# Optimization experiments

Hardware: AMD Instinct MI355X
Metric: run time of the kernel (lower is better)

Reference implementation:

```python
import jax, jax.numpy as jnp
import numpy as np

N_ATOM = 2_000_000
N_FRAG = 200_000
EPS = 1e-4


def setup_inputs() -> dict:
    key = jax.random.key(0)
    k1, k2, k3, k4, k5 = jax.random.split(key, 5)
    f_atom = jax.random.normal(k1, (N_ATOM, 3), dtype=jnp.float32)
    atom_pos = jax.random.normal(k2, (N_ATOM, 3), dtype=jnp.float32) * 5.0
    T_frag = jax.random.normal(k3, (N_FRAG, 3), dtype=jnp.float32) * 5.0
    frag_id = jax.random.randint(k4, (N_ATOM,), 0, N_FRAG, dtype=jnp.int32)
    frag_sizes = jax.random.randint(k5, (N_FRAG,), 0, 30, dtype=jnp.int32)
    return {
        "f_atom": f_atom,
        "atom_pos": atom_pos,
        "T_frag": T_frag,
        "frag_id": frag_id,
        "n_frag": N_FRAG,
        "frag_sizes": frag_sizes,
    }


def reference(f_atom, atom_pos, T_frag, frag_id, n_frag, frag_sizes):
    """Newton-Euler aggregation: per-atom forces -> fragment (v, omega)."""
    seg = lambda x: jax.ops.segment_sum(x, frag_id, num_segments=n_frag)

    # scatter_mean of forces -> translational velocity [n_frag, 3]
    counts = seg(jnp.ones((f_atom.shape[0],), dtype=f_atom.dtype))  # [n_frag]
    v_frag = seg(f_atom) / jnp.maximum(counts, 1.0)[:, None]

    # lever arms and torques
    r_arm = atom_pos - T_frag[frag_id]                 # [N_atom, 3]
    torque = seg(jnp.cross(r_arm, f_atom))            # [n_frag, 3]

    # inertia tensor: I = sum(r^2) * eye - sum(r r^T)  (+ eps regularization)
    r2 = jnp.sum(r_arm * r_arm, axis=-1)              # [N_atom]
    I_diag = seg(r2)                                   # [n_frag]
    I_off = seg(r_arm[:, :, None] * r_arm[:, None, :])  # [n_frag, 3, 3]
    eye3 = jnp.eye(3, dtype=f_atom.dtype)
    I_tensor = I_diag[:, None, None] * eye3 - I_off + EPS * eye3

    # batched 3x3 solve for angular velocity
    omega_frag = jnp.linalg.solve(I_tensor, torque[..., None])[..., 0]

    # zero omega for single-atom fragments
    single_mask = (frag_sizes <= 1)[:, None]
    omega_frag = jnp.where(single_mask, jnp.zeros_like(omega_frag), omega_frag)
    return v_frag, omega_frag
```

## Files before the change

### kernel.cpp

```cpp
#include <hip/hip_runtime.h>


#define BSHIFT 9
#define BFRAGS (1 << BSHIFT)
#define NBMAX  512
#define NACC   13

#define CHUNK     4096
#define B_THREADS 512
#define TILE_B    1024
#define R_THREADS 512
#define TILE      1024

__global__ void atom_accum_kernel(const float* __restrict__ f_atom,
                                  const float* __restrict__ atom_pos,
                                  const float* __restrict__ T_frag,
                                  const int*   __restrict__ frag_id,
                                  float* __restrict__ acc,
                                  int n_atom, int n_frag) {
    int i = blockIdx.x * blockDim.x + threadIdx.x;
    if (i >= n_atom) return;
    float fx = f_atom[3 * i + 0], fy = f_atom[3 * i + 1], fz = f_atom[3 * i + 2];
    float px = atom_pos[3 * i + 0], py = atom_pos[3 * i + 1], pz = atom_pos[3 * i + 2];
    int fid = frag_id[i];
    float rx = px - T_frag[3 * fid + 0];
    float ry = py - T_frag[3 * fid + 1];
    float rz = pz - T_frag[3 * fid + 2];
    atomicAdd(&acc[0 * n_frag + fid], 1.0f);
    atomicAdd(&acc[1 * n_frag + fid], fx);
    atomicAdd(&acc[2 * n_frag + fid], fy);
    atomicAdd(&acc[3 * n_frag + fid], fz);
    atomicAdd(&acc[4 * n_frag + fid], ry * fz - rz * fy);
    atomicAdd(&acc[5 * n_frag + fid], rz * fx - rx * fz);
    atomicAdd(&acc[6 * n_frag + fid], rx * fy - ry * fx);
    atomicAdd(&acc[7 * n_frag + fid], rx * rx);
    atomicAdd(&acc[8 * n_frag + fid], ry * ry);
    atomicAdd(&acc[9 * n_frag + fid], rz * rz);
    atomicAdd(&acc[10 * n_frag + fid], rx * ry);
    atomicAdd(&acc[11 * n_frag + fid], rx * rz);
    atomicAdd(&acc[12 * n_frag + fid], ry * rz);
}

__device__ __forceinline__ void solve_frag(const float s[NACC], int fs,
                                           float* vout, float* oout) {
    float inv_cnt = 1.0f / fmaxf(s[0], 1.0f);
    vout[0] = s[1] * inv_cnt;
    vout[1] = s[2] * inv_cnt;
    vout[2] = s[3] * inv_cnt;

    double sxx = (double)s[7], syy = (double)s[8], szz = (double)s[9];
    double sxy = (double)s[10], sxz = (double)s[11], syz = (double)s[12];
    const double eps = 1e-4;
    double d = sxx + syy + szz;
    double a00 = d - sxx + eps, a11 = d - syy + eps, a22 = d - szz + eps;
    double a01 = -sxy, a02 = -sxz, a12 = -syz;

    double c00 = a11 * a22 - a12 * a12;
    double c01 = a02 * a12 - a01 * a22;
    double c02 = a01 * a12 - a02 * a11;
    double det = a00 * c00 + a01 * c01 + a02 * c02;
    double inv_det = (det != 0.0) ? 1.0 / det : 0.0;
    double c11 = a00 * a22 - a02 * a02;
    double c12 = a01 * a02 - a00 * a12;
    double c22 = a00 * a11 - a01 * a01;

    double tx = (double)s[4], ty = (double)s[5], tz = (double)s[6];
    if (fs <= 1) {
        oout[0] = 0.0f; oout[1] = 0.0f; oout[2] = 0.0f;
    } else {
        oout[0] = (float)((c00 * tx + c01 * ty + c02 * tz) * inv_det);
        oout[1] = (float)((c01 * tx + c11 * ty + c12 * tz) * inv_det);
        oout[2] = (float)((c02 * tx + c12 * ty + c22 * tz) * inv_det);
    }
}

__global__ void finalize_accum_kernel(const float* __restrict__ acc,
                                      const int* __restrict__ frag_sizes,
                                      float* __restrict__ out, int n_frag) {
    int i = blockIdx.x * blockDim.x + threadIdx.x;
    if (i >= n_frag) return;
    float s[NACC];
#pragma unroll
    for (int c = 0; c < NACC; ++c) s[c] = acc[(size_t)c * n_frag + i];
    float v[3], o[3];
    solve_frag(s, frag_sizes[i], v, o);
    out[3 * i + 0] = v[0]; out[3 * i + 1] = v[1]; out[3 * i + 2] = v[2];
    float* om = out + 3 * (size_t)n_frag;
    om[3 * i + 0] = o[0]; om[3 * i + 1] = o[1]; om[3 * i + 2] = o[2];
}


__device__ __forceinline__ int xcd_swizzle(int orig, int n) {
    int q = n >> 3, r = n & 7;
    int xcd = orig & 7, slot = orig >> 3;
    return (xcd < r ? xcd * (q + 1) : r * (q + 1) + (xcd - r) * q) + slot;
}

__global__ __launch_bounds__(B_THREADS)
void hist_kernel(const int* __restrict__ frag_id, unsigned* __restrict__ h,
                 int n_atom, int nb) {
    __shared__ unsigned hh[NBMAX];
    int tid = threadIdx.x;
    if (tid < nb) hh[tid] = 0;
    __syncthreads();
    int c0 = blockIdx.x * CHUNK;
    int cend = min(c0 + CHUNK, n_atom);
    for (int i = c0 + tid; i < cend; i += B_THREADS)
        atomicAdd(&hh[frag_id[i] >> BSHIFT], 1u);
    __syncthreads();
    size_t row = (size_t)blockIdx.x * nb;
    if (tid < nb) h[row + tid] = hh[tid];
}

__global__ void colscan_kernel(unsigned* __restrict__ h, unsigned* __restrict__ T,
                               int nb, int nreg) {
    int wid = (blockIdx.x * blockDim.x + threadIdx.x) >> 6;
    int lane = threadIdx.x & 63;
    if (wid >= nb) return;
    unsigned run = 0;
    for (int k0 = 0; k0 < nreg; k0 += 64) {
        int k = k0 + lane;
        unsigned v = (k < nreg) ? h[(size_t)k * nb + wid] : 0u;
        unsigned incl = v;
#pragma unroll
        for (int o = 1; o < 64; o <<= 1) {
            unsigned x = __shfl_up(incl, o);
            if (lane >= o) incl += x;
        }
        if (k < nreg) h[(size_t)k * nb + wid] = run + (incl - v);
        run += __shfl(incl, 63);
    }
    if (lane == 0) T[wid] = run;
}

__global__ __launch_bounds__(1024)
void gscan_kernel(const unsigned* __restrict__ T, unsigned* __restrict__ gstart,
                  int nb) {
    __shared__ unsigned s[1024];
    int t = threadIdx.x;
    unsigned v = (t < nb) ? T[t] : 0u;
    s[t] = v;
    __syncthreads();
    for (int o = 1; o < 1024; o <<= 1) {
        unsigned x = (t >= o) ? s[t - o] : 0u;
        __syncthreads();
        s[t] += x;
        __syncthreads();
    }
    if (t < nb) gstart[t] = s[t] - v;
    if (t == 0) gstart[nb] = s[nb - 1];
}

__global__ __launch_bounds__(B_THREADS)
void build_kernel(const float* __restrict__ f_atom,
                  const float* __restrict__ atom_pos,
                  const float* __restrict__ T_frag,
                  const int* __restrict__ frag_id,
                  const unsigned* __restrict__ h,
                  const unsigned* __restrict__ gstart,
                  float* __restrict__ payload,
                  int n_atom, int nb, int nreg) {
    __shared__ float stage[TILE_B * 8];
    __shared__ unsigned cursor[NBMAX];
    __shared__ unsigned cnt[NBMAX];
    __shared__ unsigned tfs[NBMAX + 1];
    __shared__ unsigned wsum[B_THREADS / 64];

    int tid = threadIdx.x;
    int wave = tid >> 6, lane = tid & 63;
    int blk = xcd_swizzle(blockIdx.x, nreg);

    size_t row = (size_t)blk * nb;
    if (tid < nb) cursor[tid] = gstart[tid] + h[row + tid];

    int c0 = blk * CHUNK;
    int cend = min(c0 + CHUNK, n_atom);

    for (int tbase = c0; tbase < cend; tbase += TILE_B) {
        int tcount = min(TILE_B, cend - tbase);
        cnt[tid] = 0;
        __syncthreads();

        float4 p0j[2], p1j[2];
        unsigned rankj[2]; int bj[2]; bool actj[2];
#pragma unroll
        for (int j = 0; j < 2; ++j) {
            int i = tbase + tid + j * B_THREADS;
            actj[j] = (i < cend);
            bj[j] = 0; rankj[j] = 0;
            if (actj[j]) {
                int fid = frag_id[i];
                int b = fid >> BSHIFT;
                bj[j] = b;
                rankj[j] = atomicAdd(&cnt[b], 1u);
                float fx = f_atom[3 * i + 0], fy = f_atom[3 * i + 1],
                      fz = f_atom[3 * i + 2];
                float rx = atom_pos[3 * i + 0] - T_frag[3 * fid + 0];
                float ry = atom_pos[3 * i + 1] - T_frag[3 * fid + 1];
                float rz = atom_pos[3 * i + 2] - T_frag[3 * fid + 2];
                p0j[j] = make_float4(fx, fy, fz, __int_as_float(fid));
                p1j[j] = make_float4(rx, ry, rz, 0.0f);
            }
        }
        __syncthreads();

        unsigned v = cnt[tid];
        unsigned incl = v;
#pragma unroll
        for (int o = 1; o < 64; o <<= 1) {
            unsigned x = __shfl_up(incl, o);
            if (lane >= o) incl += x;
        }
        if (lane == 63) wsum[wave] = incl;
        __syncthreads();
        unsigned wbase = 0;
#pragma unroll
        for (int w = 0; w < B_THREADS / 64; ++w)
            wbase += (w < wave) ? wsum[w] : 0u;
        tfs[tid] = wbase + incl - v;
        if (tid == B_THREADS - 1) tfs[NBMAX] = wbase + incl;
        __syncthreads();

#pragma unroll
        for (int j = 0; j < 2; ++j) {
            if (actj[j]) {
                unsigned slot = tfs[bj[j]] + rankj[j];
                unsigned dst = cursor[bj[j]] + rankj[j];
                p1j[j].w = __uint_as_float(dst);
                float4* d = (float4*)&stage[(size_t)slot * 8];
                d[0] = p0j[j];
                d[1] = p1j[j];
            }
        }
        __syncthreads();

        for (int s = tid; s < tcount; s += B_THREADS) {
            const float4* q = (const float4*)&stage[(size_t)s * 8];
            float4 a = q[0];
            float4 c = q[1];
            unsigned dst = __float_as_uint(c.w);
            float4* p = (float4*)(payload + (size_t)dst * 8);
            p[0] = a;
            p[1] = c;
        }
        if (tid < nb) cursor[tid] += cnt[tid];
    }
}

__global__ __launch_bounds__(R_THREADS)
void reduce_kernel(const float* __restrict__ payload,
                   const unsigned* __restrict__ gstart,
                   const int* __restrict__ frag_sizes,
                   float* __restrict__ out, int n_frag, int nb) {
    __shared__ float stage[TILE * 8];
    __shared__ unsigned cnt[BFRAGS];
    __shared__ unsigned fstart[BFRAGS + 1];
    __shared__ unsigned wsum[R_THREADS / 64];

    int b = xcd_swizzle(blockIdx.x, nb);
    int tid = threadIdx.x;
    int wave = tid >> 6, lane = tid & 63;
    unsigned s0 = gstart[b], s1 = gstart[b + 1];

    float m0 = 0.f, m1 = 0.f, m2 = 0.f, m3 = 0.f, m4 = 0.f, m5 = 0.f,
          m6 = 0.f, m7 = 0.f, m8 = 0.f, m9 = 0.f, m10 = 0.f, m11 = 0.f,
          m12 = 0.f;

    for (unsigned tbase = s0; tbase < s1; tbase += TILE) {
        cnt[tid] = 0;
        __syncthreads();

        float4 p0j[2], p1j[2];
        unsigned rankj[2]; int lfj[2]; bool actj[2];
#pragma unroll
        for (int j = 0; j < 2; ++j) {
            unsigned s = tbase + (unsigned)tid + (unsigned)j * R_THREADS;
            actj[j] = (s < s1);
            lfj[j] = 0; rankj[j] = 0;
            if (actj[j]) {
                const float4* p = (const float4*)(payload + (size_t)s * 8);
                p0j[j] = p[0];
                p1j[j] = p[1];
                lfj[j] = __float_as_int(p0j[j].w) & (BFRAGS - 1);
                rankj[j] = atomicAdd(&cnt[lfj[j]], 1u);
            }
        }
        __syncthreads();

        unsigned v = cnt[tid];
        unsigned incl = v;
#pragma unroll
        for (int o = 1; o < 64; o <<= 1) {
            unsigned x = __shfl_up(incl, o);
            if (lane >= o) incl += x;
        }
        if (lane == 63) wsum[wave] = incl;
        __syncthreads();
        unsigned wbase = 0;
#pragma unroll
        for (int w = 0; w < R_THREADS / 64; ++w)
            wbase += (w < wave) ? wsum[w] : 0u;
        fstart[tid] = wbase + incl - v;
        if (tid == R_THREADS - 1) fstart[BFRAGS] = wbase + incl;
        __syncthreads();

#pragma unroll
        for (int j = 0; j < 2; ++j) {
            if (actj[j]) {
                unsigned slot = fstart[lfj[j]] + rankj[j];
                float4* d = (float4*)&stage[(size_t)slot * 8];
                d[0] = p0j[j];
                d[1] = p1j[j];
            }
        }
        __syncthreads();

        unsigned e0 = fstart[tid], e1 = fstart[tid + 1];
        for (unsigned u = e0; u < e1; ++u) {
            const float4* q = (const float4*)&stage[(size_t)u * 8];
            float4 a = q[0];
            float4 c = q[1];
            float fx = a.x, fy = a.y, fz = a.z;
            float rx = c.x, ry = c.y, rz = c.z;
            m0 += 1.0f;
            m1 += fx; m2 += fy; m3 += fz;
            m4 += ry * fz - rz * fy;
            m5 += rz * fx - rx * fz;
            m6 += rx * fy - ry * fx;
            m7 += rx * rx; m8 += ry * ry; m9 += rz * rz;
            m10 += rx * ry; m11 += rx * rz; m12 += ry * rz;
        }
    }

    int fid = (b << BSHIFT) + tid;
    if (fid < n_frag) {
        float sv[NACC] = {m0, m1, m2, m3, m4, m5, m6,
                          m7, m8, m9, m10, m11, m12};
        float v[3], o[3];
        solve_frag(sv, frag_sizes[fid], v, o);
        out[3 * fid + 0] = v[0];
        out[3 * fid + 1] = v[1];
        out[3 * fid + 2] = v[2];
        float* om = out + 3 * (size_t)n_frag;
        om[3 * fid + 0] = o[0];
        om[3 * fid + 1] = o[1];
        om[3 * fid + 2] = o[2];
    }
}


static inline size_t pad256(size_t x) { return (x + 255) & ~(size_t)255; }

extern "C" void kernel_launch(void* const* d_in, const int* in_sizes, int n_in,
                              void* d_out, int out_size, void* d_ws, size_t ws_size,
                              hipStream_t stream) {
    const float* f_atom   = (const float*)d_in[0];
    const float* atom_pos = (const float*)d_in[1];
    const float* T_frag   = (const float*)d_in[2];
    const int*   frag_id  = (const int*)d_in[3];
    const int*   frag_sizes = (const int*)d_in[5];

    int n_atom = in_sizes[0] / 3;
    int n_frag = in_sizes[2] / 3;
    int nb   = (n_frag + BFRAGS - 1) >> BSHIFT;
    int nreg = (n_atom + CHUNK - 1) / CHUNK;

    size_t h_bytes   = pad256((size_t)nreg * nb * sizeof(unsigned));
    size_t ctl_bytes = pad256(((size_t)nb + (size_t)nb + 1) * sizeof(unsigned));
    size_t payload_bytes = (size_t)n_atom * 8 * sizeof(float);
    bool sorted_ok = (nb <= NBMAX) &&
                     (h_bytes + ctl_bytes + payload_bytes <= ws_size);

    if (sorted_ok) {
        unsigned* h      = (unsigned*)d_ws;
        unsigned* T      = (unsigned*)((char*)d_ws + h_bytes);
        unsigned* gstart = T + nb;
        float* payload   = (float*)((char*)d_ws + h_bytes + ctl_bytes);

        hist_kernel<<<nreg, B_THREADS, 0, stream>>>(frag_id, h, n_atom, nb);
        int cs_blocks = (nb * 64 + 255) / 256;
        colscan_kernel<<<cs_blocks, 256, 0, stream>>>(h, T, nb, nreg);
        gscan_kernel<<<1, 1024, 0, stream>>>(T, gstart, nb);
        build_kernel<<<nreg, B_THREADS, 0, stream>>>(f_atom, atom_pos, T_frag,
                                                     frag_id, h, gstart, payload,
                                                     n_atom, nb, nreg);
        reduce_kernel<<<nb, R_THREADS, 0, stream>>>(payload, gstart, frag_sizes,
                                                    (float*)d_out, n_frag, nb);
    } else {
        float* acc = (float*)d_ws;
        hipMemsetAsync(acc, 0, (size_t)NACC * n_frag * sizeof(float), stream);
        int threads = 256;
        atom_accum_kernel<<<(n_atom + threads - 1) / threads, threads, 0, stream>>>(
            f_atom, atom_pos, T_frag, frag_id, acc, n_atom, n_frag);
        finalize_accum_kernel<<<(n_frag + threads - 1) / threads, threads, 0, stream>>>(
            acc, frag_sizes, (float*)d_out, n_frag);
    }
}
```

Baseline: 90.43 us.

## Widen fragment buckets to 1024 and process 1536-atom tiles in counting sort

```diff
diff --git a/kernel.cpp b/kernel.cpp
--- a/kernel.cpp
+++ b/kernel.cpp
@@ -1,16 +1,17 @@
 #include <hip/hip_runtime.h>
 
 
-#define BSHIFT 9
+#define BSHIFT 10
 #define BFRAGS (1 << BSHIFT)
-#define NBMAX  512
+#define NBMAX  256
 #define NACC   13
 
-#define CHUNK     4096
+#define TILE_B    1536
+#define NTILES    3
+#define CHUNK     (TILE_B * NTILES)
 #define B_THREADS 512
-#define TILE_B    1024
 #define R_THREADS 512
-#define TILE      1024
+#define TILE      1536
 
 __global__ void atom_accum_kernel(const float* __restrict__ f_atom,
                                   const float* __restrict__ atom_pos,
@@ -101,7 +102,7 @@
                  int n_atom, int nb) {
     __shared__ unsigned hh[NBMAX];
     int tid = threadIdx.x;
-    if (tid < nb) hh[tid] = 0;
+    if (tid < NBMAX) hh[tid] = 0;
     __syncthreads();
     int c0 = blockIdx.x * CHUNK;
     int cend = min(c0 + CHUNK, n_atom);
@@ -163,11 +164,11 @@
     __shared__ float stage[TILE_B * 8];
     __shared__ unsigned cursor[NBMAX];
     __shared__ unsigned cnt[NBMAX];
-    __shared__ unsigned tfs[NBMAX + 1];
-    __shared__ unsigned wsum[B_THREADS / 64];
+    __shared__ unsigned tfs[NBMAX];
+    __shared__ unsigned wsum[NBMAX / 64];
 
     int tid = threadIdx.x;
-    int wave = tid >> 6, lane = tid & 63;
+    int lane = tid & 63;
     int blk = xcd_swizzle(blockIdx.x, nreg);
 
     size_t row = (size_t)blk * nb;
@@ -178,13 +179,13 @@
 
     for (int tbase = c0; tbase < cend; tbase += TILE_B) {
         int tcount = min(TILE_B, cend - tbase);
-        cnt[tid] = 0;
-        __syncthreads();
-
-        float4 p0j[2], p1j[2];
-        unsigned rankj[2]; int bj[2]; bool actj[2];
-#pragma unroll
-        for (int j = 0; j < 2; ++j) {
+        if (tid < NBMAX) cnt[tid] = 0;
+        __syncthreads();
+
+        float4 p0j[3], p1j[3];
+        unsigned rankj[3]; int bj[3]; bool actj[3];
+#pragma unroll
+        for (int j = 0; j < 3; ++j) {
             int i = tbase + tid + j * B_THREADS;
             actj[j] = (i < cend);
             bj[j] = 0; rankj[j] = 0;
@@ -198,35 +199,37 @@
                 float rx = atom_pos[3 * i + 0] - T_frag[3 * fid + 0];
                 float ry = atom_pos[3 * i + 1] - T_frag[3 * fid + 1];
                 float rz = atom_pos[3 * i + 2] - T_frag[3 * fid + 2];
+                unsigned dst = cursor[b] + rankj[j];
                 p0j[j] = make_float4(fx, fy, fz, __int_as_float(fid));
-                p1j[j] = make_float4(rx, ry, rz, 0.0f);
+                p1j[j] = make_float4(rx, ry, rz, __uint_as_float(dst));
             }
         }
         __syncthreads();
 
-        unsigned v = cnt[tid];
-        unsigned incl = v;
-#pragma unroll
-        for (int o = 1; o < 64; o <<= 1) {
-            unsigned x = __shfl_up(incl, o);
-            if (lane >= o) incl += x;
-        }
-        if (lane == 63) wsum[wave] = incl;
-        __syncthreads();
-        unsigned wbase = 0;
-#pragma unroll
-        for (int w = 0; w < B_THREADS / 64; ++w)
-            wbase += (w < wave) ? wsum[w] : 0u;
-        tfs[tid] = wbase + incl - v;
-        if (tid == B_THREADS - 1) tfs[NBMAX] = wbase + incl;
-        __syncthreads();
-
-#pragma unroll
-        for (int j = 0; j < 2; ++j) {
+        if (tid < NBMAX) {
+            unsigned v = cnt[tid];
+            unsigned incl = v;
+#pragma unroll
+            for (int o = 1; o < 64; o <<= 1) {
+                unsigned x = __shfl_up(incl, o);
+                if (lane >= o) incl += x;
+            }
+            if (lane == 63) wsum[tid >> 6] = incl;
+            __syncthreads();
+            unsigned wbase = 0;
+#pragma unroll
+            for (int w = 0; w < NBMAX / 64; ++w)
+                wbase += (w < (tid >> 6)) ? wsum[w] : 0u;
+            tfs[tid] = wbase + incl - v;
+        } else {
+            __syncthreads();
+        }
+        __syncthreads();
+
+#pragma unroll
+        for (int j = 0; j < 3; ++j) {
             if (actj[j]) {
                 unsigned slot = tfs[bj[j]] + rankj[j];
-                unsigned dst = cursor[bj[j]] + rankj[j];
-                p1j[j].w = __uint_as_float(dst);
                 float4* d = (float4*)&stage[(size_t)slot * 8];
                 d[0] = p0j[j];
                 d[1] = p1j[j];
@@ -254,7 +257,6 @@
                    float* __restrict__ out, int n_frag, int nb) {
     __shared__ float stage[TILE * 8];
     __shared__ unsigned cnt[BFRAGS];
-    __shared__ unsigned fstart[BFRAGS + 1];
     __shared__ unsigned wsum[R_THREADS / 64];
 
     int b = xcd_swizzle(blockIdx.x, nb);
@@ -262,18 +264,20 @@
     int wave = tid >> 6, lane = tid & 63;
     unsigned s0 = gstart[b], s1 = gstart[b + 1];
 
-    float m0 = 0.f, m1 = 0.f, m2 = 0.f, m3 = 0.f, m4 = 0.f, m5 = 0.f,
-          m6 = 0.f, m7 = 0.f, m8 = 0.f, m9 = 0.f, m10 = 0.f, m11 = 0.f,
-          m12 = 0.f;
+    float a0 = 0.f, a1 = 0.f, a2 = 0.f, a3 = 0.f, a4 = 0.f, a5 = 0.f, a6 = 0.f,
+          a7 = 0.f, a8 = 0.f, a9 = 0.f, a10 = 0.f, a11 = 0.f, a12 = 0.f;
+    float b0 = 0.f, b1 = 0.f, b2 = 0.f, b3 = 0.f, b4 = 0.f, b5 = 0.f, b6 = 0.f,
+          b7 = 0.f, b8 = 0.f, b9 = 0.f, b10 = 0.f, b11 = 0.f, b12 = 0.f;
 
     for (unsigned tbase = s0; tbase < s1; tbase += TILE) {
         cnt[tid] = 0;
-        __syncthreads();
-
-        float4 p0j[2], p1j[2];
-        unsigned rankj[2]; int lfj[2]; bool actj[2];
-#pragma unroll
-        for (int j = 0; j < 2; ++j) {
+        cnt[tid + R_THREADS] = 0;
+        __syncthreads();
+
+        float4 p0j[3], p1j[3];
+        unsigned rankj[3]; int lfj[3]; bool actj[3];
+#pragma unroll
+        for (int j = 0; j < 3; ++j) {
             unsigned s = tbase + (unsigned)tid + (unsigned)j * R_THREADS;
             actj[j] = (s < s1);
             lfj[j] = 0; rankj[j] = 0;
@@ -287,8 +291,9 @@
         }
         __syncthreads();
 
-        unsigned v = cnt[tid];
-        unsigned incl = v;
+        unsigned v0 = cnt[2 * tid], v1 = cnt[2 * tid + 1];
+        unsigned p = v0 + v1;
+        unsigned incl = p;
 #pragma unroll
         for (int o = 1; o < 64; o <<= 1) {
             unsigned x = __shfl_up(incl, o);
@@ -300,14 +305,15 @@
 #pragma unroll
         for (int w = 0; w < R_THREADS / 64; ++w)
             wbase += (w < wave) ? wsum[w] : 0u;
-        fstart[tid] = wbase + incl - v;
-        if (tid == R_THREADS - 1) fstart[BFRAGS] = wbase + incl;
-        __syncthreads();
-
-#pragma unroll
-        for (int j = 0; j < 2; ++j) {
+        unsigned X = wbase + incl - p;
+        cnt[2 * tid] = X;
+        cnt[2 * tid + 1] = X + v0;
+        __syncthreads();
+
+#pragma unroll
+        for (int j = 0; j < 3; ++j) {
             if (actj[j]) {
-                unsigned slot = fstart[lfj[j]] + rankj[j];
+                unsigned slot = cnt[lfj[j]] + rankj[j];
                 float4* d = (float4*)&stage[(size_t)slot * 8];
                 d[0] = p0j[j];
                 d[1] = p1j[j];
@@ -315,36 +321,53 @@
         }
         __syncthreads();
 
-        unsigned e0 = fstart[tid], e1 = fstart[tid + 1];
-        for (unsigned u = e0; u < e1; ++u) {
+        for (unsigned u = X; u < X + v0; ++u) {
             const float4* q = (const float4*)&stage[(size_t)u * 8];
             float4 a = q[0];
             float4 c = q[1];
             float fx = a.x, fy = a.y, fz = a.z;
             float rx = c.x, ry = c.y, rz = c.z;
-            m0 += 1.0f;
-            m1 += fx; m2 += fy; m3 += fz;
-            m4 += ry * fz - rz * fy;
-            m5 += rz * fx - rx * fz;
-            m6 += rx * fy - ry * fx;
-            m7 += rx * rx; m8 += ry * ry; m9 += rz * rz;
-            m10 += rx * ry; m11 += rx * rz; m12 += ry * rz;
-        }
-    }
-
-    int fid = (b << BSHIFT) + tid;
-    if (fid < n_frag) {
-        float sv[NACC] = {m0, m1, m2, m3, m4, m5, m6,
-                          m7, m8, m9, m10, m11, m12};
+            a0 += 1.0f;
+            a1 += fx; a2 += fy; a3 += fz;
+            a4 += ry * fz - rz * fy;
+            a5 += rz * fx - rx * fz;
+            a6 += rx * fy - ry * fx;
+            a7 += rx * rx; a8 += ry * ry; a9 += rz * rz;
+            a10 += rx * ry; a11 += rx * rz; a12 += ry * rz;
+        }
+        for (unsigned u = X + v0; u < X + v0 + v1; ++u) {
+            const float4* q = (const float4*)&stage[(size_t)u * 8];
+            float4 a = q[0];
+            float4 c = q[1];
+            float fx = a.x, fy = a.y, fz = a.z;
+            float rx = c.x, ry = c.y, rz = c.z;
+            b0 += 1.0f;
+            b1 += fx; b2 += fy; b3 += fz;
+            b4 += ry * fz - rz * fy;
+            b5 += rz * fx - rx * fz;
+            b6 += rx * fy - ry * fx;
+            b7 += rx * rx; b8 += ry * ry; b9 += rz * rz;
+            b10 += rx * ry; b11 += rx * rz; b12 += ry * rz;
+        }
+        __syncthreads();
+    }
+
+    float* om = out + 3 * (size_t)n_frag;
+    int fidA = (b << BSHIFT) + 2 * tid;
+    if (fidA < n_frag) {
+        float sv[NACC] = {a0, a1, a2, a3, a4, a5, a6, a7, a8, a9, a10, a11, a12};
         float v[3], o[3];
-        solve_frag(sv, frag_sizes[fid], v, o);
-        out[3 * fid + 0] = v[0];
-        out[3 * fid + 1] = v[1];
-        out[3 * fid + 2] = v[2];
-        float* om = out + 3 * (size_t)n_frag;
-        om[3 * fid + 0] = o[0];
-        om[3 * fid + 1] = o[1];
-        om[3 * fid + 2] = o[2];
+        solve_frag(sv, frag_sizes[fidA], v, o);
+        out[3 * fidA + 0] = v[0]; out[3 * fidA + 1] = v[1]; out[3 * fidA + 2] = v[2];
+        om[3 * fidA + 0] = o[0]; om[3 * fidA + 1] = o[1]; om[3 * fidA + 2] = o[2];
+    }
+    int fidB = fidA + 1;
+    if (fidB < n_frag) {
+        float sv[NACC] = {b0, b1, b2, b3, b4, b5, b6, b7, b8, b9, b10, b11, b12};
+        float v[3], o[3];
+        solve_frag(sv, frag_sizes[fidB], v, o);
+        out[3 * fidB + 0] = v[0]; out[3 * fidB + 1] = v[1]; out[3 * fidB + 2] = v[2];
+        om[3 * fidB + 0] = o[0]; om[3 * fidB + 1] = o[1]; om[3 * fidB + 2] = o[2];
     }
 }
 
```

Result: slower. 93.07 us (+2.9%).
